# Optimization experiments

Hardware: AMD Instinct MI355X
Metric: run time of the kernel (lower is better)

## Reference

```python
import jax, jax.numpy as jnp
import numpy as np

N_NODES = 100000


def sage_conv(x, src, dst, Wl, bl, Wr):
    # PyG SAGEConv (aggr='mean'): out = lin_l(mean_{j in N(i)} x_j) + lin_r(x_i)
    msg = x[src]                                                   # [E, d] gather
    agg = jax.ops.segment_sum(msg, dst, num_segments=N_NODES)      # [N, d]
    cnt = jax.ops.segment_sum(jnp.ones((src.shape[0], 1), x.dtype), dst,
                              num_segments=N_NODES)                # [N, 1]
    mean = agg / jnp.maximum(cnt, 1.0)
    return mean @ Wl + bl + x @ Wr


def setup_inputs() -> dict:
    key = jax.random.key(0)
    ks = jax.random.split(key, 9)
    N, E, D_IN = N_NODES, 3200000, 64
    x = jax.random.normal(ks[0], (N, D_IN), dtype=jnp.float32)
    edge_index = jax.random.randint(ks[1], (2, E), 0, N, dtype=jnp.int64)

    def glorot(k, fan_in, fan_out):
        lim = float(np.sqrt(6.0 / (fan_in + fan_out)))
        return jax.random.uniform(k, (fan_in, fan_out), jnp.float32, -lim, lim)

    return {
        "x": x,
        "edge_index": edge_index,
        "W1l": glorot(ks[2], D_IN, 64), "b1": jnp.zeros((64,), jnp.float32),
        "W1r": glorot(ks[3], D_IN, 64),
        "W2l": glorot(ks[4], 64, 32), "b2": jnp.zeros((32,), jnp.float32),
        "W2r": glorot(ks[5], 64, 32),
        "W3l": glorot(ks[6], 32, 1), "b3": jnp.zeros((1,), jnp.float32),
        "W3r": glorot(ks[7], 32, 1),
    }


def reference(x, edge_index, W1l, b1, W1r, W2l, b2, W2r, W3l, b3, W3r):
    src, dst = edge_index[0], edge_index[1]
    h = jax.nn.relu(sage_conv(x, src, dst, W1l, b1, W1r))   # dropout: eval mode (identity)
    h = jax.nn.relu(sage_conv(h, src, dst, W2l, b2, W2r))
    h = sage_conv(h, src, dst, W3l, b3, W3r)
    return jax.nn.sigmoid(h)                                # [N, 1]
```

## Files before the change

kernel.cpp:

```cpp
#include <hip/hip_runtime.h>
#include <math.h>

#define NN 100000
#define NB 391
#define BT 8192
#define CAP 12288

typedef float vfloat2 __attribute__((ext_vector_type(2)));

__device__ __forceinline__ unsigned short f2bf(float f) {
    unsigned int u = __float_as_uint(f);
    u += 0x7fffu + ((u >> 16) & 1u);
    return (unsigned short)(u >> 16);
}
__device__ __forceinline__ float bf_lo(unsigned int p) { return __uint_as_float(p << 16); }
__device__ __forceinline__ float bf_hi(unsigned int p) { return __uint_as_float(p & 0xffff0000u); }

__device__ __forceinline__ unsigned char f2fp8(float f) {
    const int p = __builtin_amdgcn_cvt_pk_fp8_f32(f, f, 0, false);
    return (unsigned char)(p & 0xFF);
}
template <bool HI>
__device__ __forceinline__ vfloat2 fp8pk2(unsigned int w) {
    return __builtin_amdgcn_cvt_pk_f32_fp8((int)w, HI);
}

template <int D_IN, int D_OUT, int NPB, int FUSE_IN, int Y_MODE>
__global__ void __launch_bounds__(256)
mlp_dual_kernel(const float* __restrict__ in0,
                const float* __restrict__ in1,
                const float* __restrict__ Wl,
                const float* __restrict__ Wr,
                const float* __restrict__ bias,
                void* __restrict__ yout,
                float* __restrict__ zout,
                int n_nodes) {
    constexpr int COLS = 2 * D_OUT;
    constexpr int NG = 256 / COLS;
    constexpr int STR = (COLS >= 64) ? D_IN : (D_IN + 1);
    __shared__ float sh[NPB * STR];
    const int t = threadIdx.x;
    const int node0 = blockIdx.x * NPB;
    for (int i = t; i < NPB * D_IN; i += 256) {
        const int ln = i / D_IN, k = i % D_IN;
        const int n = node0 + ln;
        float v = 0.f;
        if (n < n_nodes) {
            const long long idx = (long long)n * D_IN + k;
            v = FUSE_IN ? fmaxf(in0[idx] + in1[idx], 0.f) : in0[idx];
        }
        sh[ln * STR + k] = v;
    }
    const int c = t % COLS;
    const int g = t / COLS;
    const bool left = (c < D_OUT);
    const int cc = left ? c : c - D_OUT;
    const float* Wsel = left ? Wl : Wr;
    float wcol[D_IN];
#pragma unroll
    for (int k = 0; k < D_IN; ++k) wcol[k] = Wsel[k * D_OUT + cc];
    const float badd = left ? 0.f : bias[cc];
    __syncthreads();
#pragma unroll
    for (int p = 0; p < NPB / NG; ++p) {
        const int ln = g + p * NG;
        const int n = node0 + ln;
        float acc = 0.f;
#pragma unroll
        for (int k = 0; k < D_IN; ++k) acc += sh[ln * STR + k] * wcol[k];
        if (n < n_nodes) {
            if (left) {
                if (Y_MODE == 2)      ((unsigned char*)yout)[(long long)n * D_OUT + cc] = f2fp8(acc);
                else if (Y_MODE == 1) ((unsigned short*)yout)[(long long)n * D_OUT + cc] = f2bf(acc);
                else                  ((float*)yout)[(long long)n * D_OUT + cc] = acc;
            } else {
                zout[(long long)n * D_OUT + cc] = acc + badd;
            }
        }
    }
}

__global__ void sigmoid_out_kernel(const float* __restrict__ mean,
                                   const float* __restrict__ z,
                                   float* __restrict__ out, int n) {
    const int i = blockIdx.x * 256 + threadIdx.x;
    if (i < n) out[i] = 1.0f / (1.0f + expf(-(mean[i] + z[i])));
}

__global__ void bucket_hist_kernel(const int* __restrict__ dst,
                                   int* __restrict__ bcnt, int n_edges) {
    __shared__ int lh[NB];
    for (int i = threadIdx.x; i < NB; i += 256) lh[i] = 0;
    __syncthreads();
    const int stride = gridDim.x * 256;
    for (int i = blockIdx.x * 256 + threadIdx.x; i < n_edges; i += stride)
        atomicAdd(&lh[dst[i] >> 8], 1);
    __syncthreads();
    for (int i = threadIdx.x; i < NB; i += 256)
        if (lh[i]) atomicAdd(&bcnt[i], lh[i]);
}

__global__ void __launch_bounds__(512)
bucket_scan_kernel(const int* __restrict__ bcnt, int* __restrict__ boffs,
                   int* __restrict__ bcursor) {
    __shared__ int s[512];
    const int t = threadIdx.x;
    const int v = (t < NB) ? bcnt[t] : 0;
    s[t] = v;
    __syncthreads();
    for (int off = 1; off < 512; off <<= 1) {
        const int tmp = (t >= off) ? s[t - off] : 0;
        __syncthreads();
        s[t] += tmp;
        __syncthreads();
    }
    const int excl = s[t] - v;
    if (t <= NB) boffs[t] = excl;
    if (t < NB) bcursor[t] = excl;
}

__global__ void __launch_bounds__(512)
bin_edges_kernel(const int* __restrict__ src, const int* __restrict__ dst,
                 int* __restrict__ bcursor, unsigned int* __restrict__ binned,
                 int n_edges) {
    __shared__ unsigned int stage[BT];
    __shared__ unsigned short sbkt[BT];
    __shared__ int lhist[512], lscan[512], lstart[512], gbase[512], lcur[512];
    const int t = threadIdx.x;
    const int e0 = blockIdx.x * BT;
    const int count = min(BT, n_edges - e0);
    lhist[t] = 0;
    __syncthreads();
    for (int i = t; i < count; i += 512) atomicAdd(&lhist[dst[e0 + i] >> 8], 1);
    __syncthreads();
    const int v = lhist[t];
    lscan[t] = v;
    __syncthreads();
    for (int off = 1; off < 512; off <<= 1) {
        const int tmp = (t >= off) ? lscan[t - off] : 0;
        __syncthreads();
        lscan[t] += tmp;
        __syncthreads();
    }
    const int excl = lscan[t] - v;
    lstart[t] = excl;
    lcur[t] = excl;
    if (t < NB && v > 0) gbase[t] = atomicAdd(&bcursor[t], v);
    __syncthreads();
    for (int i = t; i < count; i += 512) {
        const int d = dst[e0 + i];
        const int b = d >> 8;
        const int p = atomicAdd(&lcur[b], 1);
        stage[p] = (unsigned int)src[e0 + i] | ((unsigned int)(d & 255) << 17);
        sbkt[p] = (unsigned short)b;
    }
    __syncthreads();
    for (int i = t; i < count; i += 512) {
        const int b = sbkt[i];
        binned[gbase[b] + (i - lstart[b])] = stage[i];
    }
}

__global__ void __launch_bounds__(1024)
csr_sort_kernel(const unsigned int* __restrict__ binned,
                const int* __restrict__ boffs,
                int* __restrict__ ssrc, int* __restrict__ row_ptr,
                float* __restrict__ inv_deg, int n_nodes, int n_edges) {
    __shared__ int stage[CAP];
    __shared__ int hist[256];
    __shared__ int lexcl[256];
    __shared__ int lcur[256];
    const int t = threadIdx.x;
    const int b = blockIdx.x;
    const int s0 = boffs[b], s1 = boffs[b + 1];
    const int count = s1 - s0;
    if (t < 256) hist[t] = 0;
    __syncthreads();
    for (int i = t; i < count; i += 1024)
        atomicAdd(&hist[binned[s0 + i] >> 17], 1);
    __syncthreads();
    if (t < 256) lexcl[t] = hist[t];
    __syncthreads();
    for (int off = 1; off < 256; off <<= 1) {
        int tmp = 0;
        if (t < 256 && t >= off) tmp = lexcl[t - off];
        __syncthreads();
        if (t < 256) lexcl[t] += tmp;
        __syncthreads();
    }
    if (t < 256) {
        const int excl = lexcl[t] - hist[t];
        lcur[t] = excl;
        const int n = (b << 8) + t;
        if (n < n_nodes) {
            row_ptr[n] = s0 + excl;
            inv_deg[n] = 1.0f / (float)max(hist[t], 1);
        }
    }
    if (b == NB - 1 && t == 0) row_ptr[n_nodes] = n_edges;
    __syncthreads();
    for (int i = t; i < count; i += 1024) {
        const unsigned int v = binned[s0 + i];
        const int p = atomicAdd(&lcur[v >> 17], 1);
        if (p < CAP) stage[p] = (int)(v & 0x1FFFFu);
    }
    __syncthreads();
    for (int i = t; i < count; i += 1024) ssrc[s0 + i] = stage[i];
}

template <int D>
__global__ void agg_mean_fp8_kernel(const unsigned int* __restrict__ yb,
                                    const int* __restrict__ row_ptr,
                                    const int* __restrict__ ssrc,
                                    const float* __restrict__ inv_deg,
                                    float* __restrict__ mean, int n_nodes) {
    constexpr int G = D / 16;
    constexpr int NPB = 256 / G;
    const int g = threadIdx.x / G;
    const int lane = threadIdx.x % G;
    const int n = blockIdx.x * NPB + g;
    if (n >= n_nodes) return;
    const int s0 = row_ptr[n], s1 = row_ptr[n + 1];
    const uint4* yv = (const uint4*)yb;
    float acc[16];
#pragma unroll
    for (int i = 0; i < 16; ++i) acc[i] = 0.f;
    int e = s0;
    for (; e + 4 <= s1; e += 4) {
        uint4 v[4];
        v[0] = yv[(long long)ssrc[e] * G + lane];
        v[1] = yv[(long long)ssrc[e + 1] * G + lane];
        v[2] = yv[(long long)ssrc[e + 2] * G + lane];
        v[3] = yv[(long long)ssrc[e + 3] * G + lane];
#pragma unroll
        for (int q = 0; q < 4; ++q) {
            const unsigned int wx = v[q].x, wy = v[q].y, wz = v[q].z, ww = v[q].w;
            vfloat2 p;
            p = fp8pk2<false>(wx); acc[0]  += p.x; acc[1]  += p.y;
            p = fp8pk2<true>(wx);  acc[2]  += p.x; acc[3]  += p.y;
            p = fp8pk2<false>(wy); acc[4]  += p.x; acc[5]  += p.y;
            p = fp8pk2<true>(wy);  acc[6]  += p.x; acc[7]  += p.y;
            p = fp8pk2<false>(wz); acc[8]  += p.x; acc[9]  += p.y;
            p = fp8pk2<true>(wz);  acc[10] += p.x; acc[11] += p.y;
            p = fp8pk2<false>(ww); acc[12] += p.x; acc[13] += p.y;
            p = fp8pk2<true>(ww);  acc[14] += p.x; acc[15] += p.y;
        }
    }
    for (; e < s1; ++e) {
        const uint4 v = yv[(long long)ssrc[e] * G + lane];
        vfloat2 p;
        p = fp8pk2<false>(v.x); acc[0]  += p.x; acc[1]  += p.y;
        p = fp8pk2<true>(v.x);  acc[2]  += p.x; acc[3]  += p.y;
        p = fp8pk2<false>(v.y); acc[4]  += p.x; acc[5]  += p.y;
        p = fp8pk2<true>(v.y);  acc[6]  += p.x; acc[7]  += p.y;
        p = fp8pk2<false>(v.z); acc[8]  += p.x; acc[9]  += p.y;
        p = fp8pk2<true>(v.z);  acc[10] += p.x; acc[11] += p.y;
        p = fp8pk2<false>(v.w); acc[12] += p.x; acc[13] += p.y;
        p = fp8pk2<true>(v.w);  acc[14] += p.x; acc[15] += p.y;
    }
    const float inv = inv_deg[n];
    float4* mv = (float4*)mean;
    const long long base = (long long)n * (D / 4) + lane * 4;
#pragma unroll
    for (int q = 0; q < 4; ++q)
        mv[base + q] = make_float4(acc[4 * q] * inv, acc[4 * q + 1] * inv,
                                   acc[4 * q + 2] * inv, acc[4 * q + 3] * inv);
}

template <int D>
__global__ void agg_mean_bf16_kernel(const unsigned int* __restrict__ yb,
                                     const int* __restrict__ row_ptr,
                                     const int* __restrict__ ssrc,
                                     const float* __restrict__ inv_deg,
                                     float* __restrict__ mean, int n_nodes) {
    constexpr int G = D / 8;
    constexpr int NPB = 256 / G;
    const int g = threadIdx.x / G;
    const int lane = threadIdx.x % G;
    const int n = blockIdx.x * NPB + g;
    if (n >= n_nodes) return;
    const int s0 = row_ptr[n], s1 = row_ptr[n + 1];
    const uint4* yv = (const uint4*)yb;
    float a0 = 0.f, a1 = 0.f, a2 = 0.f, a3 = 0.f;
    float a4 = 0.f, a5 = 0.f, a6 = 0.f, a7 = 0.f;
    int e = s0;
    for (; e + 4 <= s1; e += 4) {
        const int i0 = ssrc[e], i1 = ssrc[e + 1];
        const int i2 = ssrc[e + 2], i3 = ssrc[e + 3];
        const uint4 v0 = yv[(long long)i0 * G + lane];
        const uint4 v1 = yv[(long long)i1 * G + lane];
        const uint4 v2 = yv[(long long)i2 * G + lane];
        const uint4 v3 = yv[(long long)i3 * G + lane];
        a0 += bf_lo(v0.x) + bf_lo(v1.x) + bf_lo(v2.x) + bf_lo(v3.x);
        a1 += bf_hi(v0.x) + bf_hi(v1.x) + bf_hi(v2.x) + bf_hi(v3.x);
        a2 += bf_lo(v0.y) + bf_lo(v1.y) + bf_lo(v2.y) + bf_lo(v3.y);
        a3 += bf_hi(v0.y) + bf_hi(v1.y) + bf_hi(v2.y) + bf_hi(v3.y);
        a4 += bf_lo(v0.z) + bf_lo(v1.z) + bf_lo(v2.z) + bf_lo(v3.z);
        a5 += bf_hi(v0.z) + bf_hi(v1.z) + bf_hi(v2.z) + bf_hi(v3.z);
        a6 += bf_lo(v0.w) + bf_lo(v1.w) + bf_lo(v2.w) + bf_lo(v3.w);
        a7 += bf_hi(v0.w) + bf_hi(v1.w) + bf_hi(v2.w) + bf_hi(v3.w);
    }
    for (; e < s1; ++e) {
        const uint4 v = yv[(long long)ssrc[e] * G + lane];
        a0 += bf_lo(v.x); a1 += bf_hi(v.x);
        a2 += bf_lo(v.y); a3 += bf_hi(v.y);
        a4 += bf_lo(v.z); a5 += bf_hi(v.z);
        a6 += bf_lo(v.w); a7 += bf_hi(v.w);
    }
    const float inv = inv_deg[n];
    float4* mv = (float4*)mean;
    const long long base = (long long)n * (D / 4) + lane * 2;
    mv[base]     = make_float4(a0 * inv, a1 * inv, a2 * inv, a3 * inv);
    mv[base + 1] = make_float4(a4 * inv, a5 * inv, a6 * inv, a7 * inv);
}

__global__ void agg_mean_d1_kernel(const float* __restrict__ y,
                                   const int* __restrict__ row_ptr,
                                   const int* __restrict__ ssrc,
                                   const float* __restrict__ inv_deg,
                                   float* __restrict__ mean, int n_nodes) {
    const int wave = threadIdx.x >> 6;
    const int lane = threadIdx.x & 63;
    const int n = blockIdx.x * 4 + wave;
    if (n >= n_nodes) return;
    const int s0 = row_ptr[n], s1 = row_ptr[n + 1];
    float acc = 0.f;
    for (int e = s0 + lane; e < s1; e += 64) acc += y[ssrc[e]];
    for (int off = 32; off > 0; off >>= 1) acc += __shfl_down(acc, off, 64);
    if (lane == 0) mean[n] = acc * inv_deg[n];
}

extern "C" void kernel_launch(void* const* d_in, const int* in_sizes, int n_in,
                              void* d_out, int out_size, void* d_ws, size_t ws_size,
                              hipStream_t stream) {
    const float* x = (const float*)d_in[0];
    const int* edge_index = (const int*)d_in[1];
    const float* W1l = (const float*)d_in[2];
    const float* b1  = (const float*)d_in[3];
    const float* W1r = (const float*)d_in[4];
    const float* W2l = (const float*)d_in[5];
    const float* b2  = (const float*)d_in[6];
    const float* W2r = (const float*)d_in[7];
    const float* W3l = (const float*)d_in[8];
    const float* b3  = (const float*)d_in[9];
    const float* W3r = (const float*)d_in[10];
    float* out = (float*)d_out;

    const int E = in_sizes[1] / 2;
    const int* src = edge_index;
    const int* dst = edge_index + E;

    float* bufY    = (float*)d_ws;
    float* meanB   = bufY + 32LL * NN;
    float* z1      = meanB + 64LL * NN;
    float* z2      = z1 + 64LL * NN;
    float* z3      = z2 + 32LL * NN;
    float* inv_deg = z3 + NN;
    int* bcnt      = (int*)(inv_deg + NN);
    int* boffs     = bcnt + NB;
    int* bcursor   = boffs + NB + 1;
    int* row_ptr   = bcursor + NB;
    int* ssrc      = row_ptr + NN + 1;
    unsigned int* binned = (unsigned int*)z1;

    const int ntiles = (E + BT - 1) / BT;

    (void)hipMemsetAsync(bcnt, 0, NB * sizeof(int), stream);
    bucket_hist_kernel<<<512, 256, 0, stream>>>(dst, bcnt, E);
    bucket_scan_kernel<<<1, 512, 0, stream>>>(bcnt, boffs, bcursor);
    bin_edges_kernel<<<ntiles, 512, 0, stream>>>(src, dst, bcursor, binned, E);
    csr_sort_kernel<<<NB, 1024, 0, stream>>>(binned, boffs, ssrc, row_ptr, inv_deg, NN, E);

    mlp_dual_kernel<64, 64, 16, 0, 2><<<(NN + 15) / 16, 256, 0, stream>>>(
        x, nullptr, W1l, W1r, b1, bufY, z1, NN);
    agg_mean_fp8_kernel<64><<<(NN + 63) / 64, 256, 0, stream>>>(
        (const unsigned int*)bufY, row_ptr, ssrc, inv_deg, meanB, NN);

    mlp_dual_kernel<64, 32, 16, 1, 1><<<(NN + 15) / 16, 256, 0, stream>>>(
        meanB, z1, W2l, W2r, b2, bufY, z2, NN);
    agg_mean_bf16_kernel<32><<<(NN + 63) / 64, 256, 0, stream>>>(
        (const unsigned int*)bufY, row_ptr, ssrc, inv_deg, meanB, NN);

    mlp_dual_kernel<32, 1, 128, 1, 0><<<(NN + 127) / 128, 256, 0, stream>>>(
        meanB, z2, W3l, W3r, b3, bufY, z3, NN);
    agg_mean_d1_kernel<<<(NN + 3) / 4, 256, 0, stream>>>(
        bufY, row_ptr, ssrc, inv_deg, meanB, NN);
    sigmoid_out_kernel<<<(NN + 255) / 256, 256, 0, stream>>>(meanB, z3, out, NN);
}
```

Measured before the change: 352.3 us.

## Use fp8 for layer-2 gather, merge dual-matmul columns, add dedicated layer-3 kernel

Layer 2's projected features are now stored as fp8 instead of bf16 and aggregated with the existing fp8 gather kernel, halving the bytes read per edge in the second aggregation. The dual MLP kernel now has each thread compute both the left and right outputs for one column, with float4 input loads and shared-memory reads. A new per-node kernel replaces the padded-shared-memory layer-3 path. The fp8 storage lowers precision of the layer-2 messages, which may hurt accuracy.

```diff
diff --git a/kernel.cpp b/kernel.cpp
--- a/kernel.cpp
+++ b/kernel.cpp
@@ -13,8 +13,6 @@
     u += 0x7fffu + ((u >> 16) & 1u);
     return (unsigned short)(u >> 16);
 }
-__device__ __forceinline__ float bf_lo(unsigned int p) { return __uint_as_float(p << 16); }
-__device__ __forceinline__ float bf_hi(unsigned int p) { return __uint_as_float(p & 0xffff0000u); }
 
 __device__ __forceinline__ unsigned char f2fp8(float f) {
     const int p = __builtin_amdgcn_cvt_pk_fp8_f32(f, f, 0, false);
@@ -25,59 +23,99 @@
     return __builtin_amdgcn_cvt_pk_f32_fp8((int)w, HI);
 }
 
-template <int D_IN, int D_OUT, int NPB, int FUSE_IN, int Y_MODE>
+template <int D_IN, int D_OUT, int NPB, int FUSE_IN>
 __global__ void __launch_bounds__(256)
-mlp_dual_kernel(const float* __restrict__ in0,
-                const float* __restrict__ in1,
-                const float* __restrict__ Wl,
-                const float* __restrict__ Wr,
-                const float* __restrict__ bias,
-                void* __restrict__ yout,
-                float* __restrict__ zout,
-                int n_nodes) {
-    constexpr int COLS = 2 * D_OUT;
-    constexpr int NG = 256 / COLS;
-    constexpr int STR = (COLS >= 64) ? D_IN : (D_IN + 1);
-    __shared__ float sh[NPB * STR];
+mlp12_kernel(const float* __restrict__ in0,
+             const float* __restrict__ in1,
+             const float* __restrict__ Wl,
+             const float* __restrict__ Wr,
+             const float* __restrict__ bias,
+             unsigned char* __restrict__ yout,
+             float* __restrict__ zout,
+             int n_nodes) {
+    constexpr int NG = 256 / D_OUT;
+    constexpr int KQ = D_IN / 4;
+    __shared__ float sh[NPB * D_IN];
     const int t = threadIdx.x;
     const int node0 = blockIdx.x * NPB;
-    for (int i = t; i < NPB * D_IN; i += 256) {
-        const int ln = i / D_IN, k = i % D_IN;
+    for (int i = t; i < NPB * KQ; i += 256) {
+        const int ln = i / KQ, kq = i % KQ;
         const int n = node0 + ln;
-        float v = 0.f;
+        float4 v = make_float4(0.f, 0.f, 0.f, 0.f);
         if (n < n_nodes) {
-            const long long idx = (long long)n * D_IN + k;
-            v = FUSE_IN ? fmaxf(in0[idx] + in1[idx], 0.f) : in0[idx];
-        }
-        sh[ln * STR + k] = v;
-    }
-    const int c = t % COLS;
-    const int g = t / COLS;
-    const bool left = (c < D_OUT);
-    const int cc = left ? c : c - D_OUT;
-    const float* Wsel = left ? Wl : Wr;
-    float wcol[D_IN];
-#pragma unroll
-    for (int k = 0; k < D_IN; ++k) wcol[k] = Wsel[k * D_OUT + cc];
-    const float badd = left ? 0.f : bias[cc];
+            v = ((const float4*)(in0 + (long long)n * D_IN))[kq];
+            if (FUSE_IN) {
+                const float4 w = ((const float4*)(in1 + (long long)n * D_IN))[kq];
+                v.x = fmaxf(v.x + w.x, 0.f);
+                v.y = fmaxf(v.y + w.y, 0.f);
+                v.z = fmaxf(v.z + w.z, 0.f);
+                v.w = fmaxf(v.w + w.w, 0.f);
+            }
+        }
+        ((float4*)sh)[i] = v;
+    }
+    const int cc = t % D_OUT;
+    const int g = t / D_OUT;
+    float wl[D_IN], wr[D_IN];
+#pragma unroll
+    for (int k = 0; k < D_IN; ++k) {
+        wl[k] = Wl[k * D_OUT + cc];
+        wr[k] = Wr[k * D_OUT + cc];
+    }
+    const float badd = bias[cc];
     __syncthreads();
 #pragma unroll
     for (int p = 0; p < NPB / NG; ++p) {
         const int ln = g + p * NG;
         const int n = node0 + ln;
-        float acc = 0.f;
-#pragma unroll
-        for (int k = 0; k < D_IN; ++k) acc += sh[ln * STR + k] * wcol[k];
+        const float4* row = (const float4*)(sh + ln * D_IN);
+        float accl = 0.f, accr = 0.f;
+#pragma unroll
+        for (int kq = 0; kq < KQ; ++kq) {
+            const float4 v = row[kq];
+            accl += v.x * wl[4 * kq] + v.y * wl[4 * kq + 1] +
+                    v.z * wl[4 * kq + 2] + v.w * wl[4 * kq + 3];
+            accr += v.x * wr[4 * kq] + v.y * wr[4 * kq + 1] +
+                    v.z * wr[4 * kq + 2] + v.w * wr[4 * kq + 3];
+        }
         if (n < n_nodes) {
-            if (left) {
-                if (Y_MODE == 2)      ((unsigned char*)yout)[(long long)n * D_OUT + cc] = f2fp8(acc);
-                else if (Y_MODE == 1) ((unsigned short*)yout)[(long long)n * D_OUT + cc] = f2bf(acc);
-                else                  ((float*)yout)[(long long)n * D_OUT + cc] = acc;
-            } else {
-                zout[(long long)n * D_OUT + cc] = acc + badd;
-            }
-        }
-    }
+            yout[(long long)n * D_OUT + cc] = f2fp8(accl);
+            zout[(long long)n * D_OUT + cc] = accr + badd;
+        }
+    }
+}
+
+template <int D_IN>
+__global__ void __launch_bounds__(256)
+mlp3_kernel(const float* __restrict__ mean,
+            const float* __restrict__ z,
+            const float* __restrict__ W3l,
+            const float* __restrict__ W3r,
+            const float* __restrict__ b3,
+            float* __restrict__ y,
+            float* __restrict__ z3, int n_nodes) {
+    __shared__ float swl[D_IN], swr[D_IN];
+    const int t = threadIdx.x;
+    if (t < D_IN) { swl[t] = W3l[t]; swr[t] = W3r[t]; }
+    __syncthreads();
+    const int n = blockIdx.x * 256 + t;
+    if (n >= n_nodes) return;
+    const float4* pm = (const float4*)(mean + (long long)n * D_IN);
+    const float4* pz = (const float4*)(z + (long long)n * D_IN);
+    float accl = 0.f, accr = 0.f;
+#pragma unroll
+    for (int q = 0; q < D_IN / 4; ++q) {
+        const float4 m4 = pm[q];
+        const float4 z4 = pz[q];
+        const float h0 = fmaxf(m4.x + z4.x, 0.f);
+        const float h1 = fmaxf(m4.y + z4.y, 0.f);
+        const float h2 = fmaxf(m4.z + z4.z, 0.f);
+        const float h3 = fmaxf(m4.w + z4.w, 0.f);
+        accl += h0 * swl[4 * q] + h1 * swl[4 * q + 1] + h2 * swl[4 * q + 2] + h3 * swl[4 * q + 3];
+        accr += h0 * swr[4 * q] + h1 * swr[4 * q + 1] + h2 * swr[4 * q + 2] + h3 * swr[4 * q + 3];
+    }
+    y[n] = accl;
+    z3[n] = accr + b3[0];
 }
 
 __global__ void sigmoid_out_kernel(const float* __restrict__ mean,
@@ -267,53 +305,6 @@
                                    acc[4 * q + 2] * inv, acc[4 * q + 3] * inv);
 }
 
-template <int D>
-__global__ void agg_mean_bf16_kernel(const unsigned int* __restrict__ yb,
-                                     const int* __restrict__ row_ptr,
-                                     const int* __restrict__ ssrc,
-                                     const float* __restrict__ inv_deg,
-                                     float* __restrict__ mean, int n_nodes) {
-    constexpr int G = D / 8;
-    constexpr int NPB = 256 / G;
-    const int g = threadIdx.x / G;
-    const int lane = threadIdx.x % G;
-    const int n = blockIdx.x * NPB + g;
-    if (n >= n_nodes) return;
-    const int s0 = row_ptr[n], s1 = row_ptr[n + 1];
-    const uint4* yv = (const uint4*)yb;
-    float a0 = 0.f, a1 = 0.f, a2 = 0.f, a3 = 0.f;
-    float a4 = 0.f, a5 = 0.f, a6 = 0.f, a7 = 0.f;
-    int e = s0;
-    for (; e + 4 <= s1; e += 4) {
-        const int i0 = ssrc[e], i1 = ssrc[e + 1];
-        const int i2 = ssrc[e + 2], i3 = ssrc[e + 3];
-        const uint4 v0 = yv[(long long)i0 * G + lane];
-        const uint4 v1 = yv[(long long)i1 * G + lane];
-        const uint4 v2 = yv[(long long)i2 * G + lane];
-        const uint4 v3 = yv[(long long)i3 * G + lane];
-        a0 += bf_lo(v0.x) + bf_lo(v1.x) + bf_lo(v2.x) + bf_lo(v3.x);
-        a1 += bf_hi(v0.x) + bf_hi(v1.x) + bf_hi(v2.x) + bf_hi(v3.x);
-        a2 += bf_lo(v0.y) + bf_lo(v1.y) + bf_lo(v2.y) + bf_lo(v3.y);
-        a3 += bf_hi(v0.y) + bf_hi(v1.y) + bf_hi(v2.y) + bf_hi(v3.y);
-        a4 += bf_lo(v0.z) + bf_lo(v1.z) + bf_lo(v2.z) + bf_lo(v3.z);
-        a5 += bf_hi(v0.z) + bf_hi(v1.z) + bf_hi(v2.z) + bf_hi(v3.z);
-        a6 += bf_lo(v0.w) + bf_lo(v1.w) + bf_lo(v2.w) + bf_lo(v3.w);
-        a7 += bf_hi(v0.w) + bf_hi(v1.w) + bf_hi(v2.w) + bf_hi(v3.w);
-    }
-    for (; e < s1; ++e) {
-        const uint4 v = yv[(long long)ssrc[e] * G + lane];
-        a0 += bf_lo(v.x); a1 += bf_hi(v.x);
-        a2 += bf_lo(v.y); a3 += bf_hi(v.y);
-        a4 += bf_lo(v.z); a5 += bf_hi(v.z);
-        a6 += bf_lo(v.w); a7 += bf_hi(v.w);
-    }
-    const float inv = inv_deg[n];
-    float4* mv = (float4*)mean;
-    const long long base = (long long)n * (D / 4) + lane * 2;
-    mv[base]     = make_float4(a0 * inv, a1 * inv, a2 * inv, a3 * inv);
-    mv[base + 1] = make_float4(a4 * inv, a5 * inv, a6 * inv, a7 * inv);
-}
-
 __global__ void agg_mean_d1_kernel(const float* __restrict__ y,
                                    const int* __restrict__ row_ptr,
                                    const int* __restrict__ ssrc,
@@ -371,17 +362,17 @@
     bin_edges_kernel<<<ntiles, 512, 0, stream>>>(src, dst, bcursor, binned, E);
     csr_sort_kernel<<<NB, 1024, 0, stream>>>(binned, boffs, ssrc, row_ptr, inv_deg, NN, E);
 
-    mlp_dual_kernel<64, 64, 16, 0, 2><<<(NN + 15) / 16, 256, 0, stream>>>(
-        x, nullptr, W1l, W1r, b1, bufY, z1, NN);
+    mlp12_kernel<64, 64, 16, 0><<<(NN + 15) / 16, 256, 0, stream>>>(
+        x, nullptr, W1l, W1r, b1, (unsigned char*)bufY, z1, NN);
     agg_mean_fp8_kernel<64><<<(NN + 63) / 64, 256, 0, stream>>>(
         (const unsigned int*)bufY, row_ptr, ssrc, inv_deg, meanB, NN);
 
-    mlp_dual_kernel<64, 32, 16, 1, 1><<<(NN + 15) / 16, 256, 0, stream>>>(
-        meanB, z1, W2l, W2r, b2, bufY, z2, NN);
-    agg_mean_bf16_kernel<32><<<(NN + 63) / 64, 256, 0, stream>>>(
+    mlp12_kernel<64, 32, 16, 1><<<(NN + 15) / 16, 256, 0, stream>>>(
+        meanB, z1, W2l, W2r, b2, (unsigned char*)bufY, z2, NN);
+    agg_mean_fp8_kernel<32><<<(NN + 127) / 128, 256, 0, stream>>>(
         (const unsigned int*)bufY, row_ptr, ssrc, inv_deg, meanB, NN);
 
-    mlp_dual_kernel<32, 1, 128, 1, 0><<<(NN + 127) / 128, 256, 0, stream>>>(
+    mlp3_kernel<32><<<(NN + 255) / 256, 256, 0, stream>>>(
         meanB, z2, W3l, W3r, b3, bufY, z3, NN);
     agg_mean_d1_kernel<<<(NN + 3) / 4, 256, 0, stream>>>(
         bufY, row_ptr, ssrc, inv_deg, meanB, NN);
```

New measurement: 349.1 us. No clear change (-0.9%).
